# Kernel optimization log

Measured on AMD Instinct MI355X. Metric: run time of the kernel, lower is better.

Reference implementation:

```python
import jax, jax.numpy as jnp
import numpy as np

TEMPERATURE = 0.2
LAMDA = 1.0
M, K = 8192, 128
NUM_CLASSES = 21


def setup_inputs() -> dict:
    key = jax.random.key(0)
    k1, k2 = jax.random.split(key)
    features = jax.random.normal(k1, (M, K), dtype=jnp.float32)
    labels = jax.random.randint(k2, (M,), 0, NUM_CLASSES, dtype=jnp.int64)
    return {"features": features, "labels": labels}


def reference(features, labels):
    # features: [M, K], labels: [M]
    m = features.shape[0]
    labels = labels.reshape(-1, 1)  # [M, 1]
    same = (labels == labels.T)  # [M, M] bool, positives
    not_diag = ~jnp.eye(m, dtype=bool)  # zero out self-similarity
    mask_pos = (same & not_diag).astype(features.dtype)
    mask_neg = ((~same) & not_diag).astype(features.dtype)

    similarity = jnp.matmul(features, features.T) / TEMPERATURE  # [M, M]
    sim_row_max = jax.lax.stop_gradient(jnp.max(similarity, axis=1, keepdims=True))
    exp_sim = jnp.exp(similarity - sim_row_max)  # diagonal handled via masks

    # per-row: lamda * sum over positives - sum over negatives
    log_prob = LAMDA * jnp.sum(exp_sim * mask_pos, axis=1) - jnp.sum(exp_sim * mask_neg, axis=1)
    loss = -jnp.mean(log_prob)
    return loss
```

## Files before the change

### kernel.cpp

```cpp
#include <hip/hip_runtime.h>
#include <stdint.h>


#define M_ROWS 8192
#define K_DIM  128
#define NCHUNK 8
#define CHUNK_COLS (M_ROWS / NCHUNK)
#define NT_PER_CHUNK (CHUNK_COLS / 32)
#define INV_T_LOG2E 7.213475204444817f

typedef __bf16 bf16x8 __attribute__((ext_vector_type(8)));
typedef float  f32x16 __attribute__((ext_vector_type(16)));
typedef unsigned short ushort8v __attribute__((ext_vector_type(8)));


__global__ __launch_bounds__(256) void prep_kernel(const float* __restrict__ f,
                                                   ushort8v* __restrict__ FB,
                                                   float* __restrict__ selfdot,
                                                   float* __restrict__ out) {
    const int t    = threadIdx.x;
    const int row  = blockIdx.x * 16 + (t >> 4);
    const int slot = t & 15;
    const float4 v0 = *(const float4*)(f + (size_t)row * K_DIM + slot * 8);
    const float4 v1 = *(const float4*)(f + (size_t)row * K_DIM + slot * 8 + 4);
    float x[8] = {v0.x, v0.y, v0.z, v0.w, v1.x, v1.y, v1.z, v1.w};
    ushort8v h;
    float ss = 0.f;
#pragma unroll
    for (int e = 0; e < 8; ++e) {
        uint32_t u = __builtin_bit_cast(uint32_t, x[e]);
        uint32_t r = (u + 0x7FFFu + ((u >> 16) & 1u)) >> 16;
        h[e] = (unsigned short)r;
        float b = __builtin_bit_cast(float, r << 16);
        ss += b * b;
    }
#pragma unroll
    for (int off = 1; off < 16; off <<= 1) ss += __shfl_xor(ss, off, 64);
    if (slot == 0) selfdot[row] = ss;
    const int ct = row >> 5, lm = row & 31;
    FB[(size_t)(ct * 16 + slot) * 32 + lm] = h;
    if (blockIdx.x == 0 && t == 0) out[0] = 0.f;
}

__global__ __launch_bounds__(256) void fused_kernel(const ushort8v* __restrict__ FB,
                                                    const int* __restrict__ labels,
                                                    const float* __restrict__ selfdot,
                                                    float* __restrict__ partials) {
    const int blk  = blockIdx.x;
    const int rg   = blk >> 3;
    const int ch   = blk & 7;
    const int w    = threadIdx.x >> 6;
    const int lane = threadIdx.x & 63;
    const int lm   = lane & 31;
    const int l5   = lane >> 5;
    const int row0 = rg * 128 + w * 32;
    const int ct0  = row0 >> 5;

    bf16x8 af[8];
#pragma unroll
    for (int s8 = 0; s8 < 8; ++s8)
        af[s8] = (const bf16x8&)FB[(size_t)(ct0 * 16 + s8 * 2 + l5) * 32 + lm];

    float m[16], s[16];
    float minm = 1e30f;
#pragma unroll
    for (int r = 0; r < 16; ++r) {
        m[r] = selfdot[row0 + (r & 3) + 8 * (r >> 2) + 4 * l5];
        s[r] = 0.f;
        minm = fminf(minm, m[r]);
    }

    const int ctb0 = ch * NT_PER_CHUNK;

    auto loadB = [&](int nt, bf16x8* dst) {
#pragma unroll
        for (int s8 = 0; s8 < 8; ++s8)
            dst[s8] = (const bf16x8&)FB[(size_t)((ctb0 + nt) * 16 + s8 * 2 + l5) * 32 + lm];
    };

    auto computeTile = [&](int nt, const bf16x8* bf) {
        f32x16 acc = {};
#pragma unroll
        for (int s8 = 0; s8 < 8; ++s8)
            acc = __builtin_amdgcn_mfma_f32_32x32x16_bf16(af[s8], bf[s8], acc, 0, 0, 0);
        float amax = acc[0];
#pragma unroll
        for (int r = 1; r < 16; ++r) amax = fmaxf(amax, acc[r]);
        if (__any(amax > minm - 22.f)) {
            const int jcol = (ctb0 + nt) * 32 + lm;
            const int labj = labels[jcol];
#pragma unroll
            for (int r = 0; r < 16; ++r) {
                const int grow = row0 + (r & 3) + 8 * (r >> 2) + 4 * l5;
                float d    = acc[r] - m[r];
                float sign = (labj == labels[grow]) ? 1.f : -1.f;
                if (jcol == grow) sign = 0.f;
                bool  p = d > 0.f;
                float e = exp2f(fminf(d, -d) * INV_T_LOG2E);
                float xx = p ? s[r] : sign;
                float yy = p ? sign : s[r];
                s[r] = fmaf(xx, e, yy);
                m[r] = fmaxf(m[r], acc[r]);
            }
            minm = m[0];
#pragma unroll
            for (int r = 1; r < 16; ++r) minm = fminf(minm, m[r]);
        }
    };

    bf16x8 b0[8], b1[8];
    loadB(0, b0);
    for (int nt = 0; nt < NT_PER_CHUNK; nt += 2) {
        loadB(nt + 1, b1);
        computeTile(nt, b0);
        if (nt + 2 < NT_PER_CHUNK) loadB(nt + 2, b0);
        computeTile(nt + 1, b1);
    }

#pragma unroll
    for (int off = 1; off < 32; off <<= 1) {
#pragma unroll
        for (int r = 0; r < 16; ++r) {
            float mo = __shfl_xor(m[r], off, 64);
            float so = __shfl_xor(s[r], off, 64);
            float d  = mo - m[r];
            bool  p  = d > 0.f;
            float e  = exp2f(fminf(d, -d) * INV_T_LOG2E);
            s[r] = p ? fmaf(s[r], e, so) : fmaf(so, e, s[r]);
            m[r] = fmaxf(m[r], mo);
        }
    }
    if (lm == 0) {
#pragma unroll
        for (int r = 0; r < 16; ++r) {
            const int grow = row0 + (r & 3) + 8 * (r >> 2) + 4 * l5;
            float* p = partials + ((size_t)grow * NCHUNK + ch) * 2;
            p[0] = m[r];
            p[1] = s[r];
        }
    }
}

__global__ __launch_bounds__(256) void merge_kernel(const float* __restrict__ partials,
                                                    float* __restrict__ out) {
    const int g = blockIdx.x * 256 + threadIdx.x;
    float M = -1e30f, S = 0.f;
#pragma unroll
    for (int c = 0; c < NCHUNK; ++c) {
        const float* p = partials + ((size_t)g * NCHUNK + c) * 2;
        float mo = p[0], so = p[1];
        float d  = mo - M;
        bool  pr = d > 0.f;
        float e  = exp2f(fminf(d, -d) * INV_T_LOG2E);
        S = pr ? fmaf(S, e, so) : fmaf(so, e, S);
        M = fmaxf(M, mo);
    }
    float val = -S * (1.0f / 8192.0f);
#pragma unroll
    for (int off = 1; off < 64; off <<= 1) val += __shfl_xor(val, off, 64);
    __shared__ float red[4];
    if ((threadIdx.x & 63) == 0) red[threadIdx.x >> 6] = val;
    __syncthreads();
    if (threadIdx.x == 0) atomicAdd(out, red[0] + red[1] + red[2] + red[3]);
}

extern "C" void kernel_launch(void* const* d_in, const int* in_sizes, int n_in,
                              void* d_out, int out_size, void* d_ws, size_t ws_size,
                              hipStream_t stream) {
    const float* feat   = (const float*)d_in[0];
    const int*   labels = (const int*)d_in[1];
    float*       out    = (float*)d_out;
    char*        ws     = (char*)d_ws;

    ushort8v* FB       = (ushort8v*)ws;
    float*    selfdot  = (float*)(ws + (size_t)M_ROWS * K_DIM * 2);
    float*    partials = (float*)(ws + (size_t)M_ROWS * K_DIM * 2 + M_ROWS * 4);

    prep_kernel<<<M_ROWS / 16, 256, 0, stream>>>(feat, FB, selfdot, out);
    fused_kernel<<<(M_ROWS / 128) * NCHUNK, 256, 0, stream>>>(FB, labels, selfdot, partials);
    merge_kernel<<<M_ROWS / 256, 256, 0, stream>>>(partials, out);
}
```

Measured before the change: 88.11 us.

## Switch Gram matmul to FP8 MFMA and double column chunks

Features are now quantized to FP8 instead of bf16 in the prep kernel, with a repacked layout, and the similarity tiles use the fp8 32x32x16 MFMA, which halves operand bytes and register footprint. The self-dot row max estimate is computed from the FP8-rounded values so it stays consistent with the MFMA results. The column split goes from 8 to 16 chunks, giving twice as many blocks with half the tiles each. FP8 precision is much coarser than bf16, and since values are divided by a temperature of 0.2 before exponentiation, the loss may drift from the reference tolerance.

```diff
diff --git a/kernel.cpp b/kernel.cpp
--- a/kernel.cpp
+++ b/kernel.cpp
@@ -4,62 +4,74 @@
 
 #define M_ROWS 8192
 #define K_DIM  128
-#define NCHUNK 8
+#define NCHUNK 16
 #define CHUNK_COLS (M_ROWS / NCHUNK)
 #define NT_PER_CHUNK (CHUNK_COLS / 32)
 #define INV_T_LOG2E 7.213475204444817f
 
-typedef __bf16 bf16x8 __attribute__((ext_vector_type(8)));
-typedef float  f32x16 __attribute__((ext_vector_type(16)));
-typedef unsigned short ushort8v __attribute__((ext_vector_type(8)));
+typedef float f32x16 __attribute__((ext_vector_type(16)));
+typedef long  lx2    __attribute__((ext_vector_type(2)));
 
 
+__device__ __forceinline__ float fp8_sumsq(int w) {
+    float v0 = __builtin_amdgcn_cvt_f32_fp8(w, 0);
+    float v1 = __builtin_amdgcn_cvt_f32_fp8(w, 1);
+    float v2 = __builtin_amdgcn_cvt_f32_fp8(w, 2);
+    float v3 = __builtin_amdgcn_cvt_f32_fp8(w, 3);
+    return v0 * v0 + v1 * v1 + v2 * v2 + v3 * v3;
+}
+
 __global__ __launch_bounds__(256) void prep_kernel(const float* __restrict__ f,
-                                                   ushort8v* __restrict__ FB,
+                                                   int4* __restrict__ FB8,
                                                    float* __restrict__ selfdot,
                                                    float* __restrict__ out) {
-    const int t    = threadIdx.x;
-    const int row  = blockIdx.x * 16 + (t >> 4);
-    const int slot = t & 15;
-    const float4 v0 = *(const float4*)(f + (size_t)row * K_DIM + slot * 8);
-    const float4 v1 = *(const float4*)(f + (size_t)row * K_DIM + slot * 8 + 4);
-    float x[8] = {v0.x, v0.y, v0.z, v0.w, v1.x, v1.y, v1.z, v1.w};
-    ushort8v h;
-    float ss = 0.f;
+    const int t   = threadIdx.x;
+    const int row = blockIdx.x * 32 + (t >> 3);
+    const int sub = t & 7;
+    const int sp  = sub >> 1;
+    const int l5  = sub & 1;
+    const float4* fr = (const float4*)(f + (size_t)row * K_DIM);
+    const float4 a0 = fr[8 * sp + 2 * l5];
+    const float4 a1 = fr[8 * sp + 2 * l5 + 1];
+    const float4 b0 = fr[8 * sp + 2 * l5 + 4];
+    const float4 b1 = fr[8 * sp + 2 * l5 + 5];
+    int w0 = __builtin_amdgcn_cvt_pk_fp8_f32(a0.x, a0.y, 0, false);
+    w0     = __builtin_amdgcn_cvt_pk_fp8_f32(a0.z, a0.w, w0, true);
+    int w1 = __builtin_amdgcn_cvt_pk_fp8_f32(a1.x, a1.y, 0, false);
+    w1     = __builtin_amdgcn_cvt_pk_fp8_f32(a1.z, a1.w, w1, true);
+    int w2 = __builtin_amdgcn_cvt_pk_fp8_f32(b0.x, b0.y, 0, false);
+    w2     = __builtin_amdgcn_cvt_pk_fp8_f32(b0.z, b0.w, w2, true);
+    int w3 = __builtin_amdgcn_cvt_pk_fp8_f32(b1.x, b1.y, 0, false);
+    w3     = __builtin_amdgcn_cvt_pk_fp8_f32(b1.z, b1.w, w3, true);
+    float ss = fp8_sumsq(w0) + fp8_sumsq(w1) + fp8_sumsq(w2) + fp8_sumsq(w3);
 #pragma unroll
-    for (int e = 0; e < 8; ++e) {
-        uint32_t u = __builtin_bit_cast(uint32_t, x[e]);
-        uint32_t r = (u + 0x7FFFu + ((u >> 16) & 1u)) >> 16;
-        h[e] = (unsigned short)r;
-        float b = __builtin_bit_cast(float, r << 16);
-        ss += b * b;
-    }
-#pragma unroll
-    for (int off = 1; off < 16; off <<= 1) ss += __shfl_xor(ss, off, 64);
-    if (slot == 0) selfdot[row] = ss;
+    for (int off = 1; off < 8; off <<= 1) ss += __shfl_xor(ss, off, 64);
+    if (sub == 0) selfdot[row] = ss;
     const int ct = row >> 5, lm = row & 31;
-    FB[(size_t)(ct * 16 + slot) * 32 + lm] = h;
+    int4 st = {w0, w1, w2, w3};
+    FB8[(size_t)(((ct * 4 + sp) * 2 + l5)) * 32 + lm] = st;
     if (blockIdx.x == 0 && t == 0) out[0] = 0.f;
 }
 
-__global__ __launch_bounds__(256) void fused_kernel(const ushort8v* __restrict__ FB,
+__global__ __launch_bounds__(256) void fused_kernel(const int4* __restrict__ FB8,
                                                     const int* __restrict__ labels,
                                                     const float* __restrict__ selfdot,
                                                     float* __restrict__ partials) {
     const int blk  = blockIdx.x;
-    const int rg   = blk >> 3;
-    const int ch   = blk & 7;
+    const int rg   = blk >> 4;
+    const int ch   = blk & 15;
     const int w    = threadIdx.x >> 6;
     const int lane = threadIdx.x & 63;
     const int lm   = lane & 31;
     const int l5   = lane >> 5;
     const int row0 = rg * 128 + w * 32;
     const int ct0  = row0 >> 5;
+    const lx2* FB = (const lx2*)FB8;
 
-    bf16x8 af[8];
+    lx2 af[4];
 #pragma unroll
-    for (int s8 = 0; s8 < 8; ++s8)
-        af[s8] = (const bf16x8&)FB[(size_t)(ct0 * 16 + s8 * 2 + l5) * 32 + lm];
+    for (int sp = 0; sp < 4; ++sp)
+        af[sp] = FB[(size_t)((ct0 * 4 + sp) * 2 + l5) * 32 + lm];
 
     float m[16], s[16];
     float minm = 1e30f;
@@ -72,17 +84,19 @@
 
     const int ctb0 = ch * NT_PER_CHUNK;
 
-    auto loadB = [&](int nt, bf16x8* dst) {
+    auto loadB = [&](int nt, lx2* dst) {
 #pragma unroll
-        for (int s8 = 0; s8 < 8; ++s8)
-            dst[s8] = (const bf16x8&)FB[(size_t)((ctb0 + nt) * 16 + s8 * 2 + l5) * 32 + lm];
+        for (int sp = 0; sp < 4; ++sp)
+            dst[sp] = FB[(size_t)(((ctb0 + nt) * 4 + sp) * 2 + l5) * 32 + lm];
     };
 
-    auto computeTile = [&](int nt, const bf16x8* bf) {
+    auto computeTile = [&](int nt, const lx2* bf) {
         f32x16 acc = {};
 #pragma unroll
-        for (int s8 = 0; s8 < 8; ++s8)
-            acc = __builtin_amdgcn_mfma_f32_32x32x16_bf16(af[s8], bf[s8], acc, 0, 0, 0);
+        for (int sp = 0; sp < 4; ++sp) {
+            acc = __builtin_amdgcn_mfma_f32_32x32x16_fp8_fp8(af[sp].x, bf[sp].x, acc, 0, 0, 0);
+            acc = __builtin_amdgcn_mfma_f32_32x32x16_fp8_fp8(af[sp].y, bf[sp].y, acc, 0, 0, 0);
+        }
         float amax = acc[0];
 #pragma unroll
         for (int r = 1; r < 16; ++r) amax = fmaxf(amax, acc[r]);
@@ -108,7 +122,7 @@
         }
     };
 
-    bf16x8 b0[8], b1[8];
+    lx2 b0[4], b1[4];
     loadB(0, b0);
     for (int nt = 0; nt < NT_PER_CHUNK; nt += 2) {
         loadB(nt + 1, b1);
@@ -172,11 +186,11 @@
     float*       out    = (float*)d_out;
     char*        ws     = (char*)d_ws;
 
-    ushort8v* FB       = (ushort8v*)ws;
-    float*    selfdot  = (float*)(ws + (size_t)M_ROWS * K_DIM * 2);
-    float*    partials = (float*)(ws + (size_t)M_ROWS * K_DIM * 2 + M_ROWS * 4);
+    int4*  FB8      = (int4*)ws;
+    float* selfdot  = (float*)(ws + (size_t)M_ROWS * K_DIM);
+    float* partials = (float*)(ws + (size_t)M_ROWS * K_DIM + M_ROWS * 4);
 
-    prep_kernel<<<M_ROWS / 16, 256, 0, stream>>>(feat, FB, selfdot, out);
-    fused_kernel<<<(M_ROWS / 128) * NCHUNK, 256, 0, stream>>>(FB, labels, selfdot, partials);
+    prep_kernel<<<M_ROWS / 32, 256, 0, stream>>>(feat, FB8, selfdot, out);
+    fused_kernel<<<(M_ROWS / 128) * NCHUNK, 256, 0, stream>>>(FB8, labels, selfdot, partials);
     merge_kernel<<<M_ROWS / 256, 256, 0, stream>>>(partials, out);
 }
```

Measured after the change: 88.74 us. Within noise of the previous version (+0.7%).
